# Performance work log

Measured on AMD Instinct MI355X. Metric: run time of the kernel, lower is better.

Reference implementation:

```python
import jax, jax.numpy as jnp
import numpy as np

EMBED_DIM = 1024
NUM_HEADS = 16
DIM_K = EMBED_DIM // NUM_HEADS
B, S = 2, 2048


def setup_inputs() -> dict:
    key = jax.random.key(0)
    ks = jax.random.split(key, 7)
    scale = 1.0 / np.sqrt(EMBED_DIM)
    return {
        "query": jax.random.normal(ks[0], (B, S, EMBED_DIM), dtype=jnp.float32),
        "key": jax.random.normal(ks[1], (B, S, EMBED_DIM), dtype=jnp.float32),
        "value": jax.random.normal(ks[2], (B, S, EMBED_DIM), dtype=jnp.float32),
        "Wq": jax.random.normal(ks[3], (EMBED_DIM, EMBED_DIM), dtype=jnp.float32) * scale,
        "Wk": jax.random.normal(ks[4], (EMBED_DIM, EMBED_DIM), dtype=jnp.float32) * scale,
        "Wv": jax.random.normal(ks[5], (EMBED_DIM, EMBED_DIM), dtype=jnp.float32) * scale,
        "Wo": jax.random.normal(ks[6], (EMBED_DIM, EMBED_DIM), dtype=jnp.float32) * scale,
    }


def reference(query, key, value, Wq, Wk, Wv, Wo):
    b, s, e = query.shape
    # nn.Linear: y = x @ W.T  (bias=False)
    def proj(x, W):
        y = x @ W.T  # [b, s, e]
        return y.reshape(b, -1, NUM_HEADS, DIM_K).transpose(0, 2, 1, 3)  # [b, h, s, dk]

    q = proj(query, Wq)
    k = proj(key, Wk)
    v = proj(value, Wv)

    # attention: scores = q k^T / sqrt(dk); softmax; @ v  (dropout p=0 in eval)
    scores = jnp.einsum("bhqd,bhkd->bhqk", q, k) / jnp.sqrt(jnp.float32(DIM_K))
    attn = jax.nn.softmax(scores, axis=-1)
    x = jnp.einsum("bhqk,bhkd->bhqd", attn, v)  # [b, h, s, dk]

    x = x.transpose(0, 2, 1, 3).reshape(b, -1, e)  # merge heads
    return x @ Wo.T
```

## Files before the change

kernel.cpp:

```cpp
#include <hip/hip_runtime.h>
#include <hip/hip_bf16.h>
#include <stdint.h>

#define EMBED 1024
#define NHEAD 16
#define DKD   64
#define BATCH 2
#define SEQ   2048
#define MROWS (BATCH*SEQ)

typedef __attribute__((ext_vector_type(8)))  short bf16x8;
typedef __attribute__((ext_vector_type(4)))  float f32x4;
typedef __attribute__((ext_vector_type(16))) float f32x16;
typedef unsigned short u16;
typedef unsigned int   u32;
typedef __attribute__((ext_vector_type(4))) u32 u32x4;

__device__ inline u16 f2bf(float f) {
  return __builtin_bit_cast(u16, __float2bfloat16(f));
}

__device__ inline u32 cvtpk(float lo, float hi) {
  u32 r;
  asm("v_cvt_pk_bf16_f32 %0, %1, %2" : "=v"(r) : "v"(lo), "v"(hi));
  return r;
}

__device__ inline void plswap(u32& x, u32& y) {
  asm volatile("v_permlane32_swap_b32 %0, %1" : "+v"(x), "+v"(y));
}

__device__ inline void gload_lds16(const u16* g, u16* l) {
  __builtin_amdgcn_global_load_lds(
      (const __attribute__((address_space(1))) u32*)(const void*)g,
      (__attribute__((address_space(3))) u32*)(void*)l, 16, 0, 0);
}

__global__ __launch_bounds__(256) void cast_all(
    const float* __restrict__ s0, const float* __restrict__ s1,
    const float* __restrict__ s2, const float* __restrict__ s3,
    const float* __restrict__ s4, const float* __restrict__ s5,
    const float* __restrict__ s6,
    u16* __restrict__ d0, u16* __restrict__ d1, u16* __restrict__ d2,
    u16* __restrict__ d3, u16* __restrict__ d4, u16* __restrict__ d5,
    u16* __restrict__ d6) {
  const int y = blockIdx.y;
  const float* s; u16* d; int n4;
  switch (y) {
    case 0: s = s0; d = d0; n4 = MROWS*EMBED/4; break;
    case 1: s = s1; d = d1; n4 = MROWS*EMBED/4; break;
    case 2: s = s2; d = d2; n4 = MROWS*EMBED/4; break;
    case 3: s = s3; d = d3; n4 = EMBED*EMBED/4; break;
    case 4: s = s4; d = d4; n4 = EMBED*EMBED/4; break;
    case 5: s = s5; d = d5; n4 = EMBED*EMBED/4; break;
    default: s = s6; d = d6; n4 = EMBED*EMBED/4; break;
  }
  int i = blockIdx.x * 256 + threadIdx.x;
  int stride = gridDim.x * 256;
  for (int idx = i; idx < n4; idx += stride) {
    float4 f = ((const float4*)s)[idx];
    ushort4 o;
    o.x = f2bf(f.x); o.y = f2bf(f.y); o.z = f2bf(f.z); o.w = f2bf(f.w);
    ((ushort4*)d)[idx] = o;
  }
}

__global__ __launch_bounds__(256)
void gemm_qkv(const u16* __restrict__ A0, const u16* __restrict__ A1,
              const u16* __restrict__ A2, const u16* __restrict__ B0,
              const u16* __restrict__ B1, const u16* __restrict__ B2,
              u16* __restrict__ C0, u16* __restrict__ C1, u16* __restrict__ C2) {
  constexpr int K = EMBED;
  __shared__ u16 As[128 * 32];
  __shared__ u16 Bs[128 * 32];
  const int z = blockIdx.z;
  const u16* A = (z == 0) ? A0 : (z == 1) ? A1 : A2;
  const u16* B = (z == 0) ? B0 : (z == 1) ? B1 : B2;
  u16* C       = (z == 0) ? C0 : (z == 1) ? C1 : C2;

  const int t = threadIdx.x;
  const int w = t >> 6, l = t & 63;
  const int lr = l & 15, lg = l >> 4;
  const int m0 = blockIdx.x * 128;
  const int n0 = blockIdx.y * 128;
  const int wr = (w >> 1) * 64, wc = (w & 1) * 64;

  f32x4 acc[4][4] = {};

  const int srow = t >> 2;
  const int scol = (t & 3) * 8;
  const u16* Ag = A + (size_t)(m0 + srow) * K + scol;
  const u16* Bg = B + (size_t)(n0 + srow) * K + scol;
  u16* AsW = As + w * 512;
  u16* BsW = Bs + w * 512;
  const size_t rowstep = (size_t)64 * K;

  for (int k0 = 0; k0 < K; k0 += 32) {
    gload_lds16(Ag + k0,           AsW);
    gload_lds16(Ag + k0 + rowstep, AsW + 64 * 32);
    gload_lds16(Bg + k0,           BsW);
    gload_lds16(Bg + k0 + rowstep, BsW + 64 * 32);
    __syncthreads();
    bf16x8 a[4], b[4];
#pragma unroll
    for (int r = 0; r < 4; r++)
      a[r] = *(const bf16x8*)(As + (wr + r * 16 + lr) * 32 + 8 * lg);
#pragma unroll
    for (int c = 0; c < 4; c++)
      b[c] = *(const bf16x8*)(Bs + (wc + c * 16 + lr) * 32 + 8 * lg);
#pragma unroll
    for (int r = 0; r < 4; r++)
#pragma unroll
      for (int c = 0; c < 4; c++)
        acc[r][c] = __builtin_amdgcn_mfma_f32_16x16x32_bf16(a[r], b[c], acc[r][c], 0, 0, 0);
    __syncthreads();
  }

#pragma unroll
  for (int r = 0; r < 4; r++)
#pragma unroll
    for (int c = 0; c < 4; c++)
#pragma unroll
      for (int j = 0; j < 4; j++) {
        int m = m0 + wr + r * 16 + lg * 4 + j;
        int n = n0 + wc + c * 16 + lr;
        int b_ = m >> 11, s_ = m & 2047;
        int h_ = n >> 6,  d_ = n & 63;
        u16 vv = f2bf(acc[r][c][j]);
        if (z == 2)
          C[((size_t)(b_ * NHEAD + h_) * DKD + d_) * SEQ + s_] = vv;
        else
          C[(((size_t)(b_ * NHEAD + h_) * SEQ + s_) << 6) + d_] = vv;
      }
}

__global__ __launch_bounds__(256)
void gemm_out(const u16* __restrict__ A, const u16* __restrict__ B,
              float* __restrict__ C) {
  constexpr int K = EMBED, N = EMBED;
  __shared__ u16 As[64 * 32];
  __shared__ u16 Bs[128 * 32];
  const int t = threadIdx.x;
  const int w = t >> 6, l = t & 63;
  const int lr = l & 15, lg = l >> 4;
  const int m0 = blockIdx.x * 64;
  const int n0 = blockIdx.y * 128;
  const int wr = (w >> 1) * 32, wc = (w & 1) * 64;

  f32x4 acc[2][4] = {};

  const int srow = t >> 2;
  const int scol = (t & 3) * 8;
  const u16* Ag = A + (size_t)(m0 + srow) * K + scol;
  const u16* Bg = B + (size_t)(n0 + srow) * K + scol;
  u16* AsW = As + w * 512;
  u16* BsW = Bs + w * 512;
  const size_t rowstep = (size_t)64 * K;

  for (int k0 = 0; k0 < K; k0 += 32) {
    gload_lds16(Ag + k0,           AsW);
    gload_lds16(Bg + k0,           BsW);
    gload_lds16(Bg + k0 + rowstep, BsW + 64 * 32);
    __syncthreads();
    bf16x8 a[2], b[4];
#pragma unroll
    for (int r = 0; r < 2; r++)
      a[r] = *(const bf16x8*)(As + (wr + r * 16 + lr) * 32 + 8 * lg);
#pragma unroll
    for (int c = 0; c < 4; c++)
      b[c] = *(const bf16x8*)(Bs + (wc + c * 16 + lr) * 32 + 8 * lg);
#pragma unroll
    for (int r = 0; r < 2; r++)
#pragma unroll
      for (int c = 0; c < 4; c++)
        acc[r][c] = __builtin_amdgcn_mfma_f32_16x16x32_bf16(a[r], b[c], acc[r][c], 0, 0, 0);
    __syncthreads();
  }

#pragma unroll
  for (int r = 0; r < 2; r++)
#pragma unroll
    for (int c = 0; c < 4; c++)
#pragma unroll
      for (int j = 0; j < 4; j++) {
        int m = m0 + wr + r * 16 + lg * 4 + j;
        int n = n0 + wc + c * 16 + lr;
        C[(size_t)m * N + n] = acc[r][c][j];
      }
}

__global__ __launch_bounds__(256, 2)
void attn_kernel(const u16* __restrict__ Qh, const u16* __restrict__ Kh,
                 const u16* __restrict__ Vt, u16* __restrict__ Xo) {
  __shared__ u16 KV[2][8192];
  const int t = threadIdx.x, w = t >> 6, l = t & 63;
  const int q32 = l & 31, h = l >> 5;
  const int xcd = blockIdx.x & 7;
  const int li  = blockIdx.x >> 3;
  const int bh  = xcd * 4 + (li >> 4);
  const int qblk = li & 15;
  const int b_ = bh >> 4, h_ = bh & 15;
  const size_t base = (size_t)bh * SEQ * DKD;
  const u16* Kb = Kh + base;
  const u16* Vb = Vt + base;
  constexpr int NT = SEQ / 64;
  constexpr float C2 = 0.18033688f;
  constexpr float THR = 44.0f;

  const int qrow = qblk * 128 + w * 32 + q32;
  bf16x8 qf[4];
#pragma unroll
  for (int ks = 0; ks < 4; ks++)
    qf[ks] = *(const bf16x8*)(Qh + base + (size_t)qrow * DKD + ks * 16 + h * 8);

  f32x16 acc[2] = {};
  float m2 = -1e30f, lsum = 0.f;

  auto stage = [&](int buf, int kt) {
    u16* kd = &KV[buf][0];
    u16* vd = &KV[buf][4096];
    const int rb = w * 8 + (l >> 3);
    const int sg = (l & 7) ^ (l >> 3);
#pragma unroll
    for (int ch = 0; ch < 2; ch++) {
      int row = ch * 32 + rb;
      gload_lds16(Kb + (size_t)(kt * 64 + row) * DKD + sg * 8,
                  kd + (ch * 32 + w * 8) * 64);
      gload_lds16(Vb + (size_t)row * SEQ + kt * 64 + sg * 8,
                  vd + (ch * 32 + w * 8) * 64);
    }
  };

  auto compute = [&](int buf) {
    const u16* kd = &KV[buf][0];
    const u16* vd = &KV[buf][4096];
    f32x16 s[2] = {};
#pragma unroll
    for (int c = 0; c < 2; c++) {
      int row = c * 32 + q32;
#pragma unroll
      for (int ks = 0; ks < 4; ks++) {
        bf16x8 kf = *(const bf16x8*)(kd + row * 64 + (((2 * ks + h) ^ (row & 7)) * 8));
        s[c] = __builtin_amdgcn_mfma_f32_32x32x16_bf16(kf, qf[ks], s[c], 0, 0, 0);
      }
    }
    bf16x8 vf[2][4];
#pragma unroll
    for (int dc = 0; dc < 2; dc++) {
      int row = dc * 32 + q32;
#pragma unroll
      for (int tile = 0; tile < 4; tile++)
        vf[dc][tile] = *(const bf16x8*)(vd + row * 64 + (((2 * tile + h) ^ (row & 7)) * 8));
    }
    float pm = s[0][0];
#pragma unroll
    for (int r = 1; r < 16; r++) pm = fmaxf(pm, s[0][r]);
#pragma unroll
    for (int r = 0; r < 16; r++) pm = fmaxf(pm, s[1][r]);
    if (__any(pm > m2 + THR)) {
      float pmo = __shfl_xor(pm, 32, 64);
      float mn = fmaxf(m2, fmaxf(pm, pmo));
      float al = __builtin_amdgcn_exp2f((m2 - mn) * C2);
      lsum *= al;
#pragma unroll
      for (int dc = 0; dc < 2; dc++)
#pragma unroll
        for (int r = 0; r < 16; r++) acc[dc][r] *= al;
      m2 = mn;
    }
    const float nm = -m2 * C2;
    bf16x8 pfrag[4];
    float ls = 0.f;
#pragma unroll
    for (int c = 0; c < 2; c++) {
      float p[16];
#pragma unroll
      for (int r = 0; r < 16; r++) {
        p[r] = __builtin_amdgcn_exp2f(__builtin_fmaf(s[c][r], C2, nm));
        ls += p[r];
      }
      u32 Pk[8];
#pragma unroll
      for (int i = 0; i < 8; i++) Pk[i] = cvtpk(p[2 * i], p[2 * i + 1]);
      plswap(Pk[0], Pk[2]); plswap(Pk[1], Pk[3]);
      plswap(Pk[4], Pk[6]); plswap(Pk[5], Pk[7]);
      pfrag[2 * c]     = __builtin_bit_cast(bf16x8, (u32x4){Pk[0], Pk[1], Pk[2], Pk[3]});
      pfrag[2 * c + 1] = __builtin_bit_cast(bf16x8, (u32x4){Pk[4], Pk[5], Pk[6], Pk[7]});
    }
    lsum += ls;
#pragma unroll
    for (int tile = 0; tile < 4; tile++)
#pragma unroll
      for (int dc = 0; dc < 2; dc++)
        acc[dc] = __builtin_amdgcn_mfma_f32_32x32x16_bf16(vf[dc][tile], pfrag[tile], acc[dc], 0, 0, 0);
  };

  stage(0, 0);
  __syncthreads();
  int cur = 0;
  for (int kt = 0; kt < NT; kt++) {
    if (kt + 1 < NT) stage(cur ^ 1, kt + 1);
    compute(cur);
    __syncthreads();
    cur ^= 1;
  }

  lsum += __shfl_xor(lsum, 32, 64);
  float inv = 1.0f / lsum;
  u16* orow = Xo + ((size_t)b_ * SEQ + qrow) * EMBED + h_ * DKD;
#pragma unroll
  for (int dc = 0; dc < 2; dc++)
#pragma unroll
    for (int k4 = 0; k4 < 4; k4++) {
      u32 w0 = cvtpk(acc[dc][4 * k4 + 0] * inv, acc[dc][4 * k4 + 1] * inv);
      u32 w1 = cvtpk(acc[dc][4 * k4 + 2] * inv, acc[dc][4 * k4 + 3] * inv);
      int d = dc * 32 + k4 * 8 + h * 4;
      uint2 pk; pk.x = w0; pk.y = w1;
      *(uint2*)(orow + d) = pk;
    }
}

extern "C" void kernel_launch(void* const* d_in, const int* in_sizes, int n_in,
                              void* d_out, int out_size, void* d_ws, size_t ws_size,
                              hipStream_t stream) {
  const float* q  = (const float*)d_in[0];
  const float* k  = (const float*)d_in[1];
  const float* v  = (const float*)d_in[2];
  const float* Wq = (const float*)d_in[3];
  const float* Wk = (const float*)d_in[4];
  const float* Wv = (const float*)d_in[5];
  const float* Wo = (const float*)d_in[6];

  char* ws = (char*)d_ws;
  const size_t SZ_X = (size_t)MROWS * EMBED * 2;
  const size_t SZ_W = (size_t)EMBED * EMBED * 2;
  u16* qbf  = (u16*)(ws);
  u16* kbf  = (u16*)(ws + SZ_X);
  u16* vbf  = (u16*)(ws + 2 * SZ_X);
  u16* wqb  = (u16*)(ws + 3 * SZ_X);
  u16* wkb  = (u16*)(ws + 3 * SZ_X + SZ_W);
  u16* wvb  = (u16*)(ws + 3 * SZ_X + 2 * SZ_W);
  u16* wob  = (u16*)(ws + 3 * SZ_X + 3 * SZ_W);
  u16* Qh   = (u16*)(ws + 3 * SZ_X + 4 * SZ_W);
  u16* Kh   = (u16*)(ws + 4 * SZ_X + 4 * SZ_W);
  u16* Vt   = (u16*)(ws + 5 * SZ_X + 4 * SZ_W);
  u16* Xcat = (u16*)(ws + 6 * SZ_X + 4 * SZ_W);

  cast_all<<<dim3(1024, 7), 256, 0, stream>>>(q, k, v, Wq, Wk, Wv, Wo,
                                              qbf, kbf, vbf, wqb, wkb, wvb, wob);

  gemm_qkv<<<dim3(MROWS / 128, EMBED / 128, 3), 256, 0, stream>>>(
      qbf, kbf, vbf, wqb, wkb, wvb, Qh, Kh, Vt);

  attn_kernel<<<512, 256, 0, stream>>>(Qh, Kh, Vt, Xcat);

  gemm_out<<<dim3(MROWS / 64, EMBED / 128), 256, 0, stream>>>(Xcat, wob, (float*)d_out);
}
```

Baseline: 122.4 us.

## Process two KV tiles per iteration with a four-slot LDS ring

Grows the shared-memory K/V buffer from two to four slots and has each loop iteration stage two future tiles while computing two current ones. The QK^T MFMAs for both tiles are issued before the softmax of the first, so matrix work from the second tile can overlap the exp/pack work of the first. This also halves the number of block-wide barriers per KV sweep. In exchange it doubles LDS per block and keeps two score accumulators live, which raises register pressure and risks lower occupancy or spills.

```diff
diff --git a/kernel.cpp b/kernel.cpp
--- a/kernel.cpp
+++ b/kernel.cpp
@@ -192,7 +192,7 @@
 __global__ __launch_bounds__(256, 2)
 void attn_kernel(const u16* __restrict__ Qh, const u16* __restrict__ Kh,
                  const u16* __restrict__ Vt, u16* __restrict__ Xo) {
-  __shared__ u16 KV[2][8192];
+  __shared__ u16 KV[4][8192];
   const int t = threadIdx.x, w = t >> 6, l = t & 63;
   const int q32 = l & 31, h = l >> 5;
   const int xcd = blockIdx.x & 7;
@@ -216,9 +216,9 @@
   f32x16 acc[2] = {};
   float m2 = -1e30f, lsum = 0.f;
 
-  auto stage = [&](int buf, int kt) {
-    u16* kd = &KV[buf][0];
-    u16* vd = &KV[buf][4096];
+  auto stage = [&](int slot, int kt) {
+    u16* kd = &KV[slot][0];
+    u16* vd = &KV[slot][4096];
     const int rb = w * 8 + (l >> 3);
     const int sg = (l & 7) ^ (l >> 3);
 #pragma unroll
@@ -231,10 +231,7 @@
     }
   };
 
-  auto compute = [&](int buf) {
-    const u16* kd = &KV[buf][0];
-    const u16* vd = &KV[buf][4096];
-    f32x16 s[2] = {};
+  auto qk = [&](const u16* kd, f32x16 (&s)[2]) {
 #pragma unroll
     for (int c = 0; c < 2; c++) {
       int row = c * 32 + q32;
@@ -244,7 +241,8 @@
         s[c] = __builtin_amdgcn_mfma_f32_32x32x16_bf16(kf, qf[ks], s[c], 0, 0, 0);
       }
     }
-    bf16x8 vf[2][4];
+  };
+  auto vload = [&](const u16* vd, bf16x8 (&vf)[2][4]) {
 #pragma unroll
     for (int dc = 0; dc < 2; dc++) {
       int row = dc * 32 + q32;
@@ -252,6 +250,8 @@
       for (int tile = 0; tile < 4; tile++)
         vf[dc][tile] = *(const bf16x8*)(vd + row * 64 + (((2 * tile + h) ^ (row & 7)) * 8));
     }
+  };
+  auto softmax_pack = [&](f32x16 (&s)[2], bf16x8 (&pfrag)[4]) {
     float pm = s[0][0];
 #pragma unroll
     for (int r = 1; r < 16; r++) pm = fmaxf(pm, s[0][r]);
@@ -269,7 +269,6 @@
       m2 = mn;
     }
     const float nm = -m2 * C2;
-    bf16x8 pfrag[4];
     float ls = 0.f;
 #pragma unroll
     for (int c = 0; c < 2; c++) {
@@ -288,6 +287,8 @@
       pfrag[2 * c + 1] = __builtin_bit_cast(bf16x8, (u32x4){Pk[4], Pk[5], Pk[6], Pk[7]});
     }
     lsum += ls;
+  };
+  auto pv = [&](bf16x8 (&vf)[2][4], bf16x8 (&pfrag)[4]) {
 #pragma unroll
     for (int tile = 0; tile < 4; tile++)
 #pragma unroll
@@ -296,13 +297,29 @@
   };
 
   stage(0, 0);
+  stage(1, 1);
   __syncthreads();
-  int cur = 0;
-  for (int kt = 0; kt < NT; kt++) {
-    if (kt + 1 < NT) stage(cur ^ 1, kt + 1);
-    compute(cur);
-    __syncthreads();
-    cur ^= 1;
+
+  for (int kt = 0; kt < NT; kt += 2) {
+    const int sA = kt & 3, sB = (kt + 1) & 3;
+    if (kt + 2 < NT) {
+      stage((kt + 2) & 3, kt + 2);
+      stage((kt + 3) & 3, kt + 3);
+    }
+    f32x16 scA[2] = {}, scB[2] = {};
+    qk(&KV[sA][0], scA);
+    qk(&KV[sB][0], scB);
+    bf16x8 vfA[2][4];
+    vload(&KV[sA][4096], vfA);
+    bf16x8 pfA[4];
+    softmax_pack(scA, pfA);
+    pv(vfA, pfA);
+    bf16x8 vfB[2][4];
+    vload(&KV[sB][4096], vfB);
+    bf16x8 pfB[4];
+    softmax_pack(scB, pfB);
+    pv(vfB, pfB);
+    __syncthreads();
   }
 
   lsum += __shfl_xor(lsum, 32, 64);
```

Result: no change. 121.8 us (-0.5%).
